# Performance work log

Hardware: AMD Instinct MI355X
Metric: run time of the kernel (lower is better)

The kernel has to match this reference:

```python
import jax, jax.numpy as jnp
import numpy as np

B, S, E, H, NE, K = 4, 1024, 1024, 16, 8, 2
DFF = 4 * E
DH = E // H
EPS = 1e-5


def _ln(x, g, b):
    m = jnp.mean(x, axis=-1, keepdims=True)
    v = jnp.mean(jnp.square(x - m), axis=-1, keepdims=True)
    return (x - m) * jax.lax.rsqrt(v + EPS) * g + b


def setup_inputs() -> dict:
    key = jax.random.key(0)
    ks = jax.random.split(key, 20)
    n = lambda k, sh, s: (jax.random.normal(k, sh, jnp.float32) * s)
    return {
        'x': n(ks[0], (B, S, E), 1.0),
        'ln1_g': jnp.ones((E,), jnp.float32), 'ln1_b': jnp.zeros((E,), jnp.float32),
        'wq': n(ks[1], (E, E), 0.02), 'bq': jnp.zeros((E,), jnp.float32),
        'wk': n(ks[2], (E, E), 0.02), 'bk': jnp.zeros((E,), jnp.float32),
        'wv': n(ks[3], (E, E), 0.02), 'bv': jnp.zeros((E,), jnp.float32),
        'wo': n(ks[4], (E, E), 0.02), 'bo': jnp.zeros((E,), jnp.float32),
        'ln2_g': jnp.ones((E,), jnp.float32), 'ln2_b': jnp.zeros((E,), jnp.float32),
        'sw1': n(ks[5], (E, DFF), 0.02), 'sb1': jnp.zeros((DFF,), jnp.float32),
        'sw2': n(ks[6], (DFF, E), 0.02), 'sb2': jnp.zeros((E,), jnp.float32),
        'ew1': n(ks[7], (NE, E, DFF), 0.02), 'eb1': jnp.zeros((NE, DFF), jnp.float32),
        'ew2': n(ks[8], (NE, DFF, E), 0.02), 'eb2': jnp.zeros((NE, E), jnp.float32),
        'w_gate': n(ks[9], (E, NE), 1.0),
    }


def reference(x, ln1_g, ln1_b, wq, bq, wk, bk, wv, bv, wo, bo,
              ln2_g, ln2_b, sw1, sb1, sw2, sb2, ew1, eb1, ew2, eb2, w_gate):
    # --- self-attention sublayer (eval: no dropout) ---
    res1 = x
    h = _ln(x, ln1_g, ln1_b)
    q = (h @ wq + bq).reshape(B, S, H, DH)
    k = (h @ wk + bk).reshape(B, S, H, DH)
    v = (h @ wv + bv).reshape(B, S, H, DH)
    scores = jnp.einsum('bqhd,bkhd->bhqk', q, k) / jnp.sqrt(jnp.float32(DH))
    attn = jax.nn.softmax(scores, axis=-1)
    ctx = jnp.einsum('bhqk,bkhd->bqhd', attn, v).reshape(B, S, E)
    x = res1 + (ctx @ wo + bo)

    # --- MoE sublayer ---
    res2 = x
    h2 = _ln(x, ln2_g, ln2_b)
    shared = jax.nn.gelu(h2 @ sw1 + sb1, approximate=False) @ sw2 + sb2

    # router (eval: clean logits, no noise)
    logits = h2 @ w_gate                                  # (B,S,NE)
    top_vals, top_idx = jax.lax.top_k(logits, K)          # (B,S,K)
    top_gates = jax.nn.softmax(top_vals, axis=-1)
    onehot = jax.nn.one_hot(top_idx, NE, dtype=x.dtype)   # (B,S,K,NE)
    gates = jnp.einsum('bsk,bske->bse', top_gates, onehot)
    probs = jax.nn.softmax(logits, axis=-1).reshape(-1, NE)
    P = probs.mean(0)
    f = (gates > 0).astype(x.dtype).reshape(-1, NE).mean(0)
    aux_loss = NE * jnp.sum(P * f)

    # dense all-expert compute, gated combine (matches original math)
    eh = jax.nn.gelu(jnp.einsum('bse,neh->bnsh', h2, ew1) + eb1[None, :, None, :],
                     approximate=False)
    eo = jnp.einsum('bnsh,nhe->bnse', eh, ew2) + eb2[None, :, None, :]
    expert_out = jnp.einsum('bnse,bsn->bse', eo, gates)

    return res2 + shared + expert_out, aux_loss
```

## Files before the change

### kernel.cpp

```cpp
#include <hip/hip_runtime.h>
#include <stdint.h>

#define B_    4
#define S_    1024
#define E_    1024
#define H_    16
#define NE_   8
#define DFF_  4096
#define NT_   4096
#define QS_   3072
#define ROWCAP_ 9216

typedef unsigned short u16;
typedef short bf16x8 __attribute__((ext_vector_type(8)));
typedef float f32x4 __attribute__((ext_vector_type(4)));

__device__ __forceinline__ float bf2f(u16 u){ unsigned v = ((unsigned)u) << 16; return __builtin_bit_cast(float, v); }
__device__ __forceinline__ u16 f2bf(float f){ unsigned x = __builtin_bit_cast(unsigned, f); return (u16)((x + 0x7FFFu + ((x >> 16) & 1u)) >> 16); }
__device__ __forceinline__ float gelu_f(float x){ return 0.5f * x * (1.f + erff(x * 0.70710678118f)); }

__device__ __forceinline__ void gl_lds16(const u16* g, u16* l){
  __builtin_amdgcn_global_load_lds((__attribute__((address_space(1))) void*)(const_cast<u16*>(g)),
                                   (__attribute__((address_space(3))) void*)(l), 16, 0, 0);
}

__launch_bounds__(256)
__global__ void ln_kernel(const float* __restrict__ x, const float* __restrict__ g,
                          const float* __restrict__ be, u16* __restrict__ out)
{
  const int row = blockIdx.x;
  const float4 v = ((const float4*)(x + (size_t)row * E_))[threadIdx.x];
  float s = v.x + v.y + v.z + v.w;
  #pragma unroll
  for(int mm = 32; mm >= 1; mm >>= 1) s += __shfl_xor(s, mm);
  __shared__ float red[8];
  const int wid = threadIdx.x >> 6;
  if((threadIdx.x & 63) == 0) red[wid] = s;
  __syncthreads();
  const float mean = (red[0] + red[1] + red[2] + red[3]) * (1.0f / E_);
  const float d0 = v.x - mean, d1 = v.y - mean, d2 = v.z - mean, d3 = v.w - mean;
  float q2 = d0*d0 + d1*d1 + d2*d2 + d3*d3;
  #pragma unroll
  for(int mm = 32; mm >= 1; mm >>= 1) q2 += __shfl_xor(q2, mm);
  if((threadIdx.x & 63) == 0) red[4 + wid] = q2;
  __syncthreads();
  const float var = (red[4] + red[5] + red[6] + red[7]) * (1.0f / E_);
  const float rs = rsqrtf(var + 1e-5f);
  const float4 gg = ((const float4*)g)[threadIdx.x];
  const float4 bb = ((const float4*)be)[threadIdx.x];
  ushort4 o;
  o.x = f2bf(d0 * rs * gg.x + bb.x);
  o.y = f2bf(d1 * rs * gg.y + bb.y);
  o.z = f2bf(d2 * rs * gg.z + bb.z);
  o.w = f2bf(d3 * rs * gg.w + bb.w);
  ((ushort4*)(out + (size_t)row * E_))[threadIdx.x] = o;
}

__launch_bounds__(256)
__global__ void transpose_kernel(const float* __restrict__ W, u16* __restrict__ WT, int K, int N)
{
  __shared__ __align__(16) u16 t[64][72];
  const size_t zo = (size_t)blockIdx.z * K * N;
  const int k0 = blockIdx.x * 64, n0 = blockIdx.y * 64;
  const int tid = threadIdx.x;
  const int kr = tid >> 2;
  const int nc = (tid & 3) * 4;
  #pragma unroll
  for(int p = 0; p < 4; p++){
    float4 v = *(const float4*)(W + zo + (size_t)(k0 + kr) * N + n0 + nc + p * 16);
    t[nc + p*16 + 0][kr] = f2bf(v.x);
    t[nc + p*16 + 1][kr] = f2bf(v.y);
    t[nc + p*16 + 2][kr] = f2bf(v.z);
    t[nc + p*16 + 3][kr] = f2bf(v.w);
  }
  __syncthreads();
  const int nr = tid >> 3;
  const int kg = (tid & 7) * 8;
  #pragma unroll
  for(int p = 0; p < 2; p++){
    const int nn = nr + p * 32;
    unsigned u0 = t[nn][kg+0], u1 = t[nn][kg+1], u2 = t[nn][kg+2], u3 = t[nn][kg+3];
    unsigned u4 = t[nn][kg+4], u5 = t[nn][kg+5], u6 = t[nn][kg+6], u7 = t[nn][kg+7];
    uint4 o;
    o.x = u0 | (u1 << 16); o.y = u2 | (u3 << 16); o.z = u4 | (u5 << 16); o.w = u6 | (u7 << 16);
    *(uint4*)(WT + zo + (size_t)(n0 + nn) * K + k0 + kg) = o;
  }
}

__global__ void bcat_kernel(const float* __restrict__ bq, const float* __restrict__ bk,
                            const float* __restrict__ bv, float* __restrict__ bcat)
{
  const int i = blockIdx.x * 256 + threadIdx.x;
  if(i < 1024) bcat[i] = bq[i];
  else if(i < 2048) bcat[i] = bk[i - 1024];
  else if(i < 3072) bcat[i] = bv[i - 2048];
}

template<int MODE>
__launch_bounds__(256)
__global__ void gemm_kernel(const u16* __restrict__ A, const u16* __restrict__ Bt,
                            int N, int Kd, const float* __restrict__ bias,
                            u16* __restrict__ outB)
{
  __shared__ __align__(16) u16 As0[4096], Bs0[4096], As1[4096], Bs1[4096];
  const int tid = threadIdx.x, lane = tid & 63, wid = tid >> 6;
  const int wm = wid >> 1, wn = wid & 1;
  const int tm = blockIdx.y * 128, tn = blockIdx.x * 128;

  const f32x4 zero = {0.f, 0.f, 0.f, 0.f};
  f32x4 acc[4][4];
  #pragma unroll
  for(int m = 0; m < 4; m++)
    #pragma unroll
    for(int n = 0; n < 4; n++) acc[m][n] = zero;

  const u16* gA0 = A  + (size_t)(tm + wid*32 + (lane >> 2)) * Kd + ((lane & 3) << 3);
  const u16* gA1 = gA0 + (size_t)16 * Kd;
  const u16* gB0 = Bt + (size_t)(tn + wid*32 + (lane >> 2)) * Kd + ((lane & 3) << 3);
  const u16* gB1 = gB0 + (size_t)16 * Kd;
  u16* lA0 = As0 + wid*1024; u16* lA1 = lA0 + 512;
  u16* lB0 = Bs0 + wid*1024; u16* lB1 = lB0 + 512;
  u16* lA0b = As1 + wid*1024; u16* lA1b = lA0b + 512;
  u16* lB0b = Bs1 + wid*1024; u16* lB1b = lB0b + 512;

  for(int k0 = 0; k0 < Kd; k0 += 64){
    __syncthreads();
    gl_lds16(gA0 + k0, lA0);  gl_lds16(gA1 + k0, lA1);
    gl_lds16(gB0 + k0, lB0);  gl_lds16(gB1 + k0, lB1);
    gl_lds16(gA0 + k0+32, lA0b); gl_lds16(gA1 + k0+32, lA1b);
    gl_lds16(gB0 + k0+32, lB0b); gl_lds16(gB1 + k0+32, lB1b);
    __syncthreads();
    bf16x8 aF[4], bF[4];
    #pragma unroll
    for(int m = 0; m < 4; m++) aF[m] = *(const bf16x8*)(As0 + (wm*64 + m*16 + (lane & 15)) * 32 + ((lane >> 4) << 3));
    #pragma unroll
    for(int n = 0; n < 4; n++) bF[n] = *(const bf16x8*)(Bs0 + (wn*64 + n*16 + (lane & 15)) * 32 + ((lane >> 4) << 3));
    #pragma unroll
    for(int m = 0; m < 4; m++)
      #pragma unroll
      for(int n = 0; n < 4; n++)
        acc[m][n] = __builtin_amdgcn_mfma_f32_16x16x32_bf16(aF[m], bF[n], acc[m][n], 0, 0, 0);
    #pragma unroll
    for(int m = 0; m < 4; m++) aF[m] = *(const bf16x8*)(As1 + (wm*64 + m*16 + (lane & 15)) * 32 + ((lane >> 4) << 3));
    #pragma unroll
    for(int n = 0; n < 4; n++) bF[n] = *(const bf16x8*)(Bs1 + (wn*64 + n*16 + (lane & 15)) * 32 + ((lane >> 4) << 3));
    #pragma unroll
    for(int m = 0; m < 4; m++)
      #pragma unroll
      for(int n = 0; n < 4; n++)
        acc[m][n] = __builtin_amdgcn_mfma_f32_16x16x32_bf16(aF[m], bF[n], acc[m][n], 0, 0, 0);
  }

  #pragma unroll
  for(int m = 0; m < 4; m++){
    const int row = tm + wm*64 + m*16 + ((lane >> 4) << 2);
    #pragma unroll
    for(int n = 0; n < 4; n++){
      const int col = tn + wn*64 + n*16 + (lane & 15);
      const float bc = bias[col];
      #pragma unroll
      for(int r = 0; r < 4; r++){
        const float v = acc[m][n][r] + bc;
        const size_t idx = (size_t)(row + r) * N + col;
        if constexpr(MODE == 0) outB[idx] = f2bf(v);
        else outB[idx] = f2bf(gelu_f(v));
      }
    }
  }
}

template<int MODE>
__launch_bounds__(256)
__global__ void gemm64_kernel(const u16* __restrict__ A, const u16* __restrict__ Bt,
                              int N, int Kd, const float* __restrict__ bias,
                              float* __restrict__ outF, const float* __restrict__ resid)
{
  __shared__ __align__(16) u16 As0[2048], As1[2048], Bs0[4096], Bs1[4096];
  const int tid = threadIdx.x, lane = tid & 63, wid = tid >> 6;
  const int wm = wid >> 1, wn = wid & 1;
  const int tm = blockIdx.y * 64, tn = blockIdx.x * 128;

  const f32x4 zero = {0.f, 0.f, 0.f, 0.f};
  f32x4 acc[2][4];
  #pragma unroll
  for(int m = 0; m < 2; m++)
    #pragma unroll
    for(int n = 0; n < 4; n++) acc[m][n] = zero;

  const u16* gA = A + (size_t)(tm + wid*16 + (lane >> 2)) * Kd + ((lane & 3) << 3);
  const u16* gB0 = Bt + (size_t)(tn + wid*32 + (lane >> 2)) * Kd + ((lane & 3) << 3);
  const u16* gB1 = gB0 + (size_t)16 * Kd;
  u16* lA  = As0 + wid*512;  u16* lAb = As1 + wid*512;
  u16* lB0 = Bs0 + wid*1024; u16* lB1 = lB0 + 512;
  u16* lB0b = Bs1 + wid*1024; u16* lB1b = lB0b + 512;

  for(int k0 = 0; k0 < Kd; k0 += 64){
    __syncthreads();
    gl_lds16(gA + k0, lA);
    gl_lds16(gB0 + k0, lB0); gl_lds16(gB1 + k0, lB1);
    gl_lds16(gA + k0+32, lAb);
    gl_lds16(gB0 + k0+32, lB0b); gl_lds16(gB1 + k0+32, lB1b);
    __syncthreads();
    bf16x8 aF[2], bF[4];
    #pragma unroll
    for(int m = 0; m < 2; m++) aF[m] = *(const bf16x8*)(As0 + (wm*32 + m*16 + (lane & 15)) * 32 + ((lane >> 4) << 3));
    #pragma unroll
    for(int n = 0; n < 4; n++) bF[n] = *(const bf16x8*)(Bs0 + (wn*64 + n*16 + (lane & 15)) * 32 + ((lane >> 4) << 3));
    #pragma unroll
    for(int m = 0; m < 2; m++)
      #pragma unroll
      for(int n = 0; n < 4; n++)
        acc[m][n] = __builtin_amdgcn_mfma_f32_16x16x32_bf16(aF[m], bF[n], acc[m][n], 0, 0, 0);
    #pragma unroll
    for(int m = 0; m < 2; m++) aF[m] = *(const bf16x8*)(As1 + (wm*32 + m*16 + (lane & 15)) * 32 + ((lane >> 4) << 3));
    #pragma unroll
    for(int n = 0; n < 4; n++) bF[n] = *(const bf16x8*)(Bs1 + (wn*64 + n*16 + (lane & 15)) * 32 + ((lane >> 4) << 3));
    #pragma unroll
    for(int m = 0; m < 2; m++)
      #pragma unroll
      for(int n = 0; n < 4; n++)
        acc[m][n] = __builtin_amdgcn_mfma_f32_16x16x32_bf16(aF[m], bF[n], acc[m][n], 0, 0, 0);
  }

  #pragma unroll
  for(int m = 0; m < 2; m++){
    const int row = tm + wm*32 + m*16 + ((lane >> 4) << 2);
    #pragma unroll
    for(int n = 0; n < 4; n++){
      const int col = tn + wn*64 + n*16 + (lane & 15);
      const float bc = bias[col];
      #pragma unroll
      for(int r = 0; r < 4; r++){
        const float v = acc[m][n][r] + bc;
        const size_t idx = (size_t)(row + r) * N + col;
        if constexpr(MODE == 2) outF[idx] = resid[idx] + v;
        else outF[idx] += v;
      }
    }
  }
}

__launch_bounds__(256)
__global__ void attn_kernel(const u16* __restrict__ qkv, u16* __restrict__ ctx)
{
  __shared__ __align__(16) u16 Ks[64 * 64];
  __shared__ __align__(16) u16 Vt[64 * 72];
  __shared__ __align__(16) u16 Ps[64 * 72];
  const int tid = threadIdx.x, lane = tid & 63, wid = tid >> 6;
  const int bh = blockIdx.y, bb = bh >> 4, hh = bh & 15;
  const int q0 = blockIdx.x * 64;
  const size_t tok0 = (size_t)bb * S_;
  const int hcol = hh * 64;

  bf16x8 aQ0, aQ1;
  {
    const u16* qp = qkv + (tok0 + q0 + wid*16 + (lane & 15)) * QS_ + hcol + ((lane >> 4) << 3);
    aQ0 = *(const bf16x8*)qp;
    aQ1 = *(const bf16x8*)(qp + 32);
  }
  const f32x4 zero = {0.f, 0.f, 0.f, 0.f};
  f32x4 accO[4]; float mrow[4], lrow[4];
  #pragma unroll
  for(int n = 0; n < 4; n++) accO[n] = zero;
  #pragma unroll
  for(int r = 0; r < 4; r++){ mrow[r] = -1e30f; lrow[r] = 0.f; }
  const float sc = 0.125f * 1.44269504f;

  for(int kv0 = 0; kv0 < S_; kv0 += 64){
    __syncthreads();
    {
      const u16* gp = qkv + (tok0 + kv0 + wid*16 + (lane >> 3)) * QS_ + 1024 + hcol + ((lane & 7) << 3);
      gl_lds16(gp, Ks + (wid*16) * 64);
      gl_lds16(gp + (size_t)8 * QS_, Ks + (wid*16 + 8) * 64);
    }
    {
      #pragma unroll
      for(int i = 0; i < 2; i++){
        const int tok = (tid >> 3) + i * 32;
        const int d0 = (tid & 7) << 3;
        bf16x8 vv = *(const bf16x8*)(qkv + (tok0 + kv0 + tok) * QS_ + 2048 + hcol + d0);
        #pragma unroll
        for(int j = 0; j < 8; j++) Vt[(d0 + j) * 72 + tok] = (u16)vv[j];
      }
    }
    __syncthreads();
    f32x4 sf[4];
    #pragma unroll
    for(int n = 0; n < 4; n++){
      bf16x8 b0 = *(const bf16x8*)(Ks + (n*16 + (lane & 15)) * 64 + ((lane >> 4) << 3));
      bf16x8 b1 = *(const bf16x8*)(Ks + (n*16 + (lane & 15)) * 64 + 32 + ((lane >> 4) << 3));
      f32x4 t = zero;
      t = __builtin_amdgcn_mfma_f32_16x16x32_bf16(aQ0, b0, t, 0, 0, 0);
      t = __builtin_amdgcn_mfma_f32_16x16x32_bf16(aQ1, b1, t, 0, 0, 0);
      sf[n] = t;
    }
    #pragma unroll
    for(int r = 0; r < 4; r++){
      const float s0 = sf[0][r]*sc, s1 = sf[1][r]*sc, s2 = sf[2][r]*sc, s3 = sf[3][r]*sc;
      float mx = fmaxf(fmaxf(s0, s1), fmaxf(s2, s3));
      #pragma unroll
      for(int mm = 1; mm < 16; mm <<= 1) mx = fmaxf(mx, __shfl_xor(mx, mm));
      const float mnew = fmaxf(mrow[r], mx);
      const float resc = exp2f(mrow[r] - mnew);
      mrow[r] = mnew;
      const float p0 = exp2f(s0 - mnew), p1 = exp2f(s1 - mnew);
      const float p2 = exp2f(s2 - mnew), p3 = exp2f(s3 - mnew);
      float ps = p0 + p1 + p2 + p3;
      #pragma unroll
      for(int mm = 1; mm < 16; mm <<= 1) ps += __shfl_xor(ps, mm);
      lrow[r] = lrow[r] * resc + ps;
      #pragma unroll
      for(int n = 0; n < 4; n++) accO[n][r] *= resc;
      const int prow = wid*16 + ((lane >> 4) << 2) + r;
      Ps[prow*72 +      (lane & 15)] = f2bf(p0);
      Ps[prow*72 + 16 + (lane & 15)] = f2bf(p1);
      Ps[prow*72 + 32 + (lane & 15)] = f2bf(p2);
      Ps[prow*72 + 48 + (lane & 15)] = f2bf(p3);
    }
    bf16x8 pa0 = *(const bf16x8*)(Ps + (wid*16 + (lane & 15)) * 72 + ((lane >> 4) << 3));
    bf16x8 pa1 = *(const bf16x8*)(Ps + (wid*16 + (lane & 15)) * 72 + 32 + ((lane >> 4) << 3));
    #pragma unroll
    for(int n = 0; n < 4; n++){
      bf16x8 b0 = *(const bf16x8*)(Vt + (n*16 + (lane & 15)) * 72 + ((lane >> 4) << 3));
      bf16x8 b1 = *(const bf16x8*)(Vt + (n*16 + (lane & 15)) * 72 + 32 + ((lane >> 4) << 3));
      accO[n] = __builtin_amdgcn_mfma_f32_16x16x32_bf16(pa0, b0, accO[n], 0, 0, 0);
      accO[n] = __builtin_amdgcn_mfma_f32_16x16x32_bf16(pa1, b1, accO[n], 0, 0, 0);
    }
  }
  const size_t cbase = tok0 * E_ + hcol;
  #pragma unroll
  for(int n = 0; n < 4; n++)
    #pragma unroll
    for(int r = 0; r < 4; r++){
      const int row = q0 + wid*16 + ((lane >> 4) << 2) + r;
      const int col = n*16 + (lane & 15);
      ctx[cbase + (size_t)row * E_ + col] = f2bf(accO[n][r] / lrow[r]);
    }
}

__launch_bounds__(256)
__global__ void router_kernel(const u16* __restrict__ h2, const float* __restrict__ wg,
                              float* __restrict__ probs, float* __restrict__ tkgate,
                              int* __restrict__ tkidx, int* __restrict__ counts)
{
  const int tok = blockIdx.x * 4 + (threadIdx.x >> 6);
  const int lane = threadIdx.x & 63;
  const u16* hr = h2 + (size_t)tok * E_;
  float a0=0,a1=0,a2=0,a3=0,a4=0,a5=0,a6=0,a7=0;
  for(int i0 = lane * 8; i0 < E_; i0 += 512){
    bf16x8 hv = *(const bf16x8*)(hr + i0);
    #pragma unroll
    for(int j = 0; j < 8; j++){
      const float hx = bf2f((u16)hv[j]);
      const float* wr = wg + (size_t)(i0 + j) * NE_;
      float4 w0 = *(const float4*)wr;
      float4 w1 = *(const float4*)(wr + 4);
      a0 += hx*w0.x; a1 += hx*w0.y; a2 += hx*w0.z; a3 += hx*w0.w;
      a4 += hx*w1.x; a5 += hx*w1.y; a6 += hx*w1.z; a7 += hx*w1.w;
    }
  }
  #pragma unroll
  for(int mm = 1; mm < 64; mm <<= 1){
    a0 += __shfl_xor(a0, mm); a1 += __shfl_xor(a1, mm); a2 += __shfl_xor(a2, mm); a3 += __shfl_xor(a3, mm);
    a4 += __shfl_xor(a4, mm); a5 += __shfl_xor(a5, mm); a6 += __shfl_xor(a6, mm); a7 += __shfl_xor(a7, mm);
  }
  if(lane == 0){
    float lg[8] = {a0,a1,a2,a3,a4,a5,a6,a7};
    float mx = lg[0];
    #pragma unroll
    for(int e = 1; e < 8; e++) mx = fmaxf(mx, lg[e]);
    float se = 0.f, ex[8];
    #pragma unroll
    for(int e = 0; e < 8; e++){ ex[e] = expf(lg[e] - mx); se += ex[e]; }
    const float inv = 1.f / se;
    float* pr = probs + (size_t)tok * 8;
    #pragma unroll
    for(int e = 0; e < 8; e++) pr[e] = ex[e] * inv;
    int i1 = 0; float v1 = lg[0];
    #pragma unroll
    for(int e = 1; e < 8; e++) if(lg[e] > v1){ v1 = lg[e]; i1 = e; }
    int i2 = -1; float v2 = -3.4e38f;
    #pragma unroll
    for(int e = 0; e < 8; e++) if(e != i1 && lg[e] > v2){ v2 = lg[e]; i2 = e; }
    const float t = expf(v2 - v1);
    tkidx[tok*2] = i1; tkidx[tok*2+1] = i2;
    tkgate[tok*2] = 1.f / (1.f + t); tkgate[tok*2+1] = t / (1.f + t);
    atomicAdd(&counts[i1], 1); atomicAdd(&counts[i2], 1);
  }
}

__global__ void init_kernel(int* __restrict__ counts, int* __restrict__ rowlist)
{
  const int t = blockIdx.x * 256 + threadIdx.x;
  if(t < 16) counts[t] = 0;
  if(t < ROWCAP_) rowlist[t] = -1;
}

__global__ void scan_kernel(const int* __restrict__ counts, int* __restrict__ aoff, int* __restrict__ cursor)
{
  if(threadIdx.x == 0){
    int o = 0;
    for(int e = 0; e < 8; e++){
      aoff[e] = o; cursor[e] = o;
      o += ((counts[e] + 127) >> 7) << 7;
    }
    aoff[8] = o;
  }
}

__global__ void build_kernel(const int* __restrict__ tkidx, const float* __restrict__ tkgate,
                             int* __restrict__ cursor, int* __restrict__ rowlist, float* __restrict__ rowgate)
{
  const int t = blockIdx.x * 256 + threadIdx.x;
  if(t >= NT_) return;
  #pragma unroll
  for(int kk = 0; kk < 2; kk++){
    const int e = tkidx[t*2 + kk];
    const int pos = atomicAdd(&cursor[e], 1);
    rowlist[pos] = t; rowgate[pos] = tkgate[t*2 + kk];
  }
}

__launch_bounds__(256)
__global__ void egemm1_kernel(const u16* __restrict__ Ah2, const u16* __restrict__ ewT,
                              const float* __restrict__ eb1,
                              const int* __restrict__ rowlist, const int* __restrict__ aoff,
                              u16* __restrict__ ehid)
{
  const int rowTile = blockIdx.y * 128;
  if(rowTile >= aoff[8]) return;
  int e = 0;
  #pragma unroll
  for(int i = 1; i < 8; i++) if(rowTile >= aoff[i]) e = i;
  __shared__ __align__(16) u16 As0[4096], Bs0[4096], As1[4096], Bs1[4096];
  const int tid = threadIdx.x, lane = tid & 63, wid = tid >> 6;
  const int wm = wid >> 1, wn = wid & 1;
  const int tn = blockIdx.x * 128;
  const u16* Bt = ewT + (size_t)e * DFF_ * E_;

  const int r0 = rowTile + wid*32 + (lane >> 2);
  int t0 = rowlist[r0];      if(t0 < 0) t0 = 0;
  int t1 = rowlist[r0 + 16]; if(t1 < 0) t1 = 0;
  const u16* gA0 = Ah2 + (size_t)t0 * E_ + ((lane & 3) << 3);
  const u16* gA1 = Ah2 + (size_t)t1 * E_ + ((lane & 3) << 3);
  const u16* gB0 = Bt + (size_t)(tn + wid*32 + (lane >> 2)) * E_ + ((lane & 3) << 3);
  const u16* gB1 = gB0 + (size_t)16 * E_;
  u16* lA0 = As0 + wid*1024; u16* lA1 = lA0 + 512;
  u16* lB0 = Bs0 + wid*1024; u16* lB1 = lB0 + 512;
  u16* lA0b = As1 + wid*1024; u16* lA1b = lA0b + 512;
  u16* lB0b = Bs1 + wid*1024; u16* lB1b = lB0b + 512;

  const f32x4 zero = {0.f,0.f,0.f,0.f};
  f32x4 acc[4][4];
  #pragma unroll
  for(int m = 0; m < 4; m++)
    #pragma unroll
    for(int n = 0; n < 4; n++) acc[m][n] = zero;

  for(int k0 = 0; k0 < E_; k0 += 64){
    __syncthreads();
    gl_lds16(gA0 + k0, lA0);  gl_lds16(gA1 + k0, lA1);
    gl_lds16(gB0 + k0, lB0);  gl_lds16(gB1 + k0, lB1);
    gl_lds16(gA0 + k0+32, lA0b); gl_lds16(gA1 + k0+32, lA1b);
    gl_lds16(gB0 + k0+32, lB0b); gl_lds16(gB1 + k0+32, lB1b);
    __syncthreads();
    bf16x8 aF[4], bF[4];
    #pragma unroll
    for(int m = 0; m < 4; m++) aF[m] = *(const bf16x8*)(As0 + (wm*64 + m*16 + (lane & 15)) * 32 + ((lane >> 4) << 3));
    #pragma unroll
    for(int n = 0; n < 4; n++) bF[n] = *(const bf16x8*)(Bs0 + (wn*64 + n*16 + (lane & 15)) * 32 + ((lane >> 4) << 3));
    #pragma unroll
    for(int m = 0; m < 4; m++)
      #pragma unroll
      for(int n = 0; n < 4; n++)
        acc[m][n] = __builtin_amdgcn_mfma_f32_16x16x32_bf16(aF[m], bF[n], acc[m][n], 0, 0, 0);
    #pragma unroll
    for(int m = 0; m < 4; m++) aF[m] = *(const bf16x8*)(As1 + (wm*64 + m*16 + (lane & 15)) * 32 + ((lane >> 4) << 3));
    #pragma unroll
    for(int n = 0; n < 4; n++) bF[n] = *(const bf16x8*)(Bs1 + (wn*64 + n*16 + (lane & 15)) * 32 + ((lane >> 4) << 3));
    #pragma unroll
    for(int m = 0; m < 4; m++)
      #pragma unroll
      for(int n = 0; n < 4; n++)
        acc[m][n] = __builtin_amdgcn_mfma_f32_16x16x32_bf16(aF[m], bF[n], acc[m][n], 0, 0, 0);
  }
  #pragma unroll
  for(int m = 0; m < 4; m++){
    const int row = rowTile + wm*64 + m*16 + ((lane >> 4) << 2);
    #pragma unroll
    for(int n = 0; n < 4; n++){
      const int col = tn + wn*64 + n*16 + (lane & 15);
      const float bc = eb1[e * DFF_ + col];
      #pragma unroll
      for(int r = 0; r < 4; r++)
        ehid[(size_t)(row + r) * DFF_ + col] = f2bf(gelu_f(acc[m][n][r] + bc));
    }
  }
}

__launch_bounds__(256)
__global__ void egemm2_kernel(const u16* __restrict__ ehid, const u16* __restrict__ ewT2,
                              const float* __restrict__ eb2,
                              const int* __restrict__ rowlist, const float* __restrict__ rowgate,
                              const int* __restrict__ aoff, float* __restrict__ outF)
{
  const int rowTile = blockIdx.y * 64;
  if(rowTile >= aoff[8]) return;
  int e = 0;
  #pragma unroll
  for(int i = 1; i < 8; i++) if(rowTile >= aoff[i]) e = i;
  __shared__ __align__(16) u16 As0[2048], As1[2048], Bs0[4096], Bs1[4096];
  const int tid = threadIdx.x, lane = tid & 63, wid = tid >> 6;
  const int wm = wid >> 1, wn = wid & 1;
  const int tn = blockIdx.x * 128;
  const u16* Bt = ewT2 + (size_t)e * E_ * DFF_;

  const u16* gA = ehid + (size_t)(rowTile + wid*16 + (lane >> 2)) * DFF_ + ((lane & 3) << 3);
  const u16* gB0 = Bt + (size_t)(tn + wid*32 + (lane >> 2)) * DFF_ + ((lane & 3) << 3);
  const u16* gB1 = gB0 + (size_t)16 * DFF_;
  u16* lA  = As0 + wid*512;  u16* lAb = As1 + wid*512;
  u16* lB0 = Bs0 + wid*1024; u16* lB1 = lB0 + 512;
  u16* lB0b = Bs1 + wid*1024; u16* lB1b = lB0b + 512;

  const f32x4 zero = {0.f,0.f,0.f,0.f};
  f32x4 acc[2][4];
  #pragma unroll
  for(int m = 0; m < 2; m++)
    #pragma unroll
    for(int n = 0; n < 4; n++) acc[m][n] = zero;

  for(int k0 = 0; k0 < DFF_; k0 += 64){
    __syncthreads();
    gl_lds16(gA + k0, lA);
    gl_lds16(gB0 + k0, lB0); gl_lds16(gB1 + k0, lB1);
    gl_lds16(gA + k0+32, lAb);
    gl_lds16(gB0 + k0+32, lB0b); gl_lds16(gB1 + k0+32, lB1b);
    __syncthreads();
    bf16x8 aF[2], bF[4];
    #pragma unroll
    for(int m = 0; m < 2; m++) aF[m] = *(const bf16x8*)(As0 + (wm*32 + m*16 + (lane & 15)) * 32 + ((lane >> 4) << 3));
    #pragma unroll
    for(int n = 0; n < 4; n++) bF[n] = *(const bf16x8*)(Bs0 + (wn*64 + n*16 + (lane & 15)) * 32 + ((lane >> 4) << 3));
    #pragma unroll
    for(int m = 0; m < 2; m++)
      #pragma unroll
      for(int n = 0; n < 4; n++)
        acc[m][n] = __builtin_amdgcn_mfma_f32_16x16x32_bf16(aF[m], bF[n], acc[m][n], 0, 0, 0);
    #pragma unroll
    for(int m = 0; m < 2; m++) aF[m] = *(const bf16x8*)(As1 + (wm*32 + m*16 + (lane & 15)) * 32 + ((lane >> 4) << 3));
    #pragma unroll
    for(int n = 0; n < 4; n++) bF[n] = *(const bf16x8*)(Bs1 + (wn*64 + n*16 + (lane & 15)) * 32 + ((lane >> 4) << 3));
    #pragma unroll
    for(int m = 0; m < 2; m++)
      #pragma unroll
      for(int n = 0; n < 4; n++)
        acc[m][n] = __builtin_amdgcn_mfma_f32_16x16x32_bf16(aF[m], bF[n], acc[m][n], 0, 0, 0);
  }
  #pragma unroll
  for(int m = 0; m < 2; m++){
    const int row = rowTile + wm*32 + m*16 + ((lane >> 4) << 2);
    #pragma unroll
    for(int r = 0; r < 4; r++){
      const int rr = row + r;
      const int tok = rowlist[rr];
      if(tok < 0) continue;
      const float g = rowgate[rr];
      #pragma unroll
      for(int n = 0; n < 4; n++){
        const int col = tn + wn*64 + n*16 + (lane & 15);
        atomicAdd(&outF[(size_t)tok * E_ + col], g * (acc[m][n][r] + eb2[e * E_ + col]));
      }
    }
  }
}

__launch_bounds__(256)
__global__ void aux_kernel(const float* __restrict__ probs, const int* __restrict__ counts,
                           float* __restrict__ outaux)
{
  float a[8];
  #pragma unroll
  for(int e = 0; e < 8; e++) a[e] = 0.f;
  for(int t = threadIdx.x; t < NT_; t += 256){
    const float* p = probs + (size_t)t * 8;
    #pragma unroll
    for(int e = 0; e < 8; e++) a[e] += p[e];
  }
  #pragma unroll
  for(int mm = 1; mm < 64; mm <<= 1)
    #pragma unroll
    for(int e = 0; e < 8; e++) a[e] += __shfl_xor(a[e], mm);
  __shared__ float part[4][8];
  const int wid = threadIdx.x >> 6;
  if((threadIdx.x & 63) == 0)
    for(int e = 0; e < 8; e++) part[wid][e] = a[e];
  __syncthreads();
  if(threadIdx.x == 0){
    float aux = 0.f;
    for(int e = 0; e < 8; e++){
      const float P = (part[0][e] + part[1][e] + part[2][e] + part[3][e]) / (float)NT_;
      const float f = (float)counts[e] / (float)NT_;
      aux += P * f;
    }
    outaux[0] = (float)NE_ * aux;
  }
}

extern "C" void kernel_launch(void* const* d_in, const int* in_sizes, int n_in,
                              void* d_out, int out_size, void* d_ws, size_t ws_size,
                              hipStream_t stream)
{
  (void)in_sizes; (void)n_in; (void)out_size; (void)ws_size;
  const float* x    = (const float*)d_in[0];
  const float* ln1g = (const float*)d_in[1];
  const float* ln1b = (const float*)d_in[2];
  const float* wq   = (const float*)d_in[3];
  const float* bq   = (const float*)d_in[4];
  const float* wk   = (const float*)d_in[5];
  const float* bk   = (const float*)d_in[6];
  const float* wv   = (const float*)d_in[7];
  const float* bv   = (const float*)d_in[8];
  const float* wo   = (const float*)d_in[9];
  const float* bo   = (const float*)d_in[10];
  const float* ln2g = (const float*)d_in[11];
  const float* ln2b = (const float*)d_in[12];
  const float* sw1  = (const float*)d_in[13];
  const float* sb1  = (const float*)d_in[14];
  const float* sw2  = (const float*)d_in[15];
  const float* sb2  = (const float*)d_in[16];
  const float* ew1  = (const float*)d_in[17];
  const float* eb1  = (const float*)d_in[18];
  const float* ew2  = (const float*)d_in[19];
  const float* eb2  = (const float*)d_in[20];
  const float* wgate= (const float*)d_in[21];
  float* out = (float*)d_out;
  char* ws = (char*)d_ws;

  const size_t MB = 1024ull * 1024ull;
  u16* h     = (u16*)(ws + 0);
  u16* h2    = (u16*)(ws + 8*MB);
  u16* wT    = (u16*)(ws + 16*MB);
  char* rt   = ws + 24*MB;
  float* probs   = (float*)(rt);
  float* tkgate  = (float*)(rt + 128*1024);
  int*   tkidx   = (int*)  (rt + 160*1024);
  int*   counts  = (int*)  (rt + 192*1024);
  int*   aoff    = (int*)  (rt + 192*1024 + 64);
  int*   cursor  = (int*)  (rt + 192*1024 + 128);
  int*   rowlist = (int*)  (rt + 256*1024);
  float* rowgate = (float*)(rt + 296*1024);
  float* bcat    = (float*)(rt + 512*1024);
  u16* qkvb  = (u16*)(ws + 32*MB);
  u16* ctx   = (u16*)(ws + 56*MB);
  u16* hidS  = (u16*)(ws + 64*MB);
  u16* ewT   = (u16*)(ws + 32*MB);
  u16* ehid  = (u16*)(ws + 96*MB);

  ln_kernel<<<NT_, 256, 0, stream>>>(x, ln1g, ln1b, h);
  bcat_kernel<<<12, 256, 0, stream>>>(bq, bk, bv, bcat);
  transpose_kernel<<<dim3(16,16,1), 256, 0, stream>>>(wq, wT,                 E_, E_);
  transpose_kernel<<<dim3(16,16,1), 256, 0, stream>>>(wk, wT + 1024*1024,     E_, E_);
  transpose_kernel<<<dim3(16,16,1), 256, 0, stream>>>(wv, wT + 2*1024*1024,   E_, E_);
  gemm_kernel<0><<<dim3(24,32), 256, 0, stream>>>(h, wT, QS_, E_, bcat, qkvb);
  attn_kernel<<<dim3(16,64), 256, 0, stream>>>(qkvb, ctx);
  transpose_kernel<<<dim3(16,16,1), 256, 0, stream>>>(wo, wT, E_, E_);
  gemm64_kernel<2><<<dim3(8,64), 256, 0, stream>>>(ctx, wT, E_, E_, bo, out, x);

  ln_kernel<<<NT_, 256, 0, stream>>>(out, ln2g, ln2b, h2);
  transpose_kernel<<<dim3(16,64,1), 256, 0, stream>>>(sw1, wT, E_, DFF_);
  gemm_kernel<1><<<dim3(32,32), 256, 0, stream>>>(h2, wT, DFF_, E_, sb1, hidS);
  transpose_kernel<<<dim3(64,16,1), 256, 0, stream>>>(sw2, wT, DFF_, E_);
  gemm64_kernel<3><<<dim3(8,64), 256, 0, stream>>>(hidS, wT, E_, DFF_, sb2, out, nullptr);

  init_kernel<<<36, 256, 0, stream>>>(counts, rowlist);
  router_kernel<<<1024, 256, 0, stream>>>(h2, wgate, probs, tkgate, tkidx, counts);
  scan_kernel<<<1, 64, 0, stream>>>(counts, aoff, cursor);
  build_kernel<<<16, 256, 0, stream>>>(tkidx, tkgate, cursor, rowlist, rowgate);

  transpose_kernel<<<dim3(16,64,8), 256, 0, stream>>>(ew1, ewT, E_, DFF_);
  egemm1_kernel<<<dim3(32,72), 256, 0, stream>>>(h2, ewT, eb1, rowlist, aoff, ehid);
  transpose_kernel<<<dim3(64,16,8), 256, 0, stream>>>(ew2, ewT, DFF_, E_);
  egemm2_kernel<<<dim3(8,144), 256, 0, stream>>>(ehid, ewT, eb2, rowlist, rowgate, aoff, out);

  aux_kernel<<<1, 256, 0, stream>>>(probs, counts, out + (size_t)NT_ * E_);
}
```

Before: 858.4 us.

## Double-buffer GEMM K-tiles with prefetch, XOR-swizzle LDS, fold init into prep

All four GEMM kernels move from loading two 32-wide K slices and then computing, with two barriers per step, to a ping-pong scheme. The next 32-wide K tile is prefetched into the alternate LDS buffer while the current one feeds the MFMAs, leaving one barrier per step. The global-to-LDS column offsets and the fragment reads get an XOR swizzle to reduce LDS bank conflicts, and the attention K tile gets the same treatment. The init kernel is merged into the bias-concat kernel, saving one launch. Correctness depends on the async global_load_lds finishing before the next iteration's barrier, with no explicit wait other than __syncthreads.

```diff
diff --git a/kernel.cpp b/kernel.cpp
--- a/kernel.cpp
+++ b/kernel.cpp
@@ -23,6 +23,9 @@
   __builtin_amdgcn_global_load_lds((__attribute__((address_space(1))) void*)(const_cast<u16*>(g)),
                                    (__attribute__((address_space(3))) void*)(l), 16, 0, 0);
 }
+
+#define KSW32(l)   ((((l) & 3) ^ (((l) >> 3) & 3)) << 3)
+#define FRAGOFF(l) (((l) & 15) * 32 + (((((l) >> 4) ^ (((l) >> 1) & 3))) << 3))
 
 __launch_bounds__(256)
 __global__ void ln_kernel(const float* __restrict__ x, const float* __restrict__ g,
@@ -87,13 +90,16 @@
   }
 }
 
-__global__ void bcat_kernel(const float* __restrict__ bq, const float* __restrict__ bk,
-                            const float* __restrict__ bv, float* __restrict__ bcat)
+__global__ void prep_kernel(const float* __restrict__ bq, const float* __restrict__ bk,
+                            const float* __restrict__ bv, float* __restrict__ bcat,
+                            int* __restrict__ counts, int* __restrict__ rowlist)
 {
   const int i = blockIdx.x * 256 + threadIdx.x;
   if(i < 1024) bcat[i] = bq[i];
   else if(i < 2048) bcat[i] = bk[i - 1024];
   else if(i < 3072) bcat[i] = bv[i - 2048];
+  if(i < 16) counts[i] = 0;
+  if(i < ROWCAP_) rowlist[i] = -1;
 }
 
 template<int MODE>
@@ -102,7 +108,7 @@
                             int N, int Kd, const float* __restrict__ bias,
                             u16* __restrict__ outB)
 {
-  __shared__ __align__(16) u16 As0[4096], Bs0[4096], As1[4096], Bs1[4096];
+  __shared__ __align__(16) u16 As[2][4096], Bs[2][4096];
   const int tid = threadIdx.x, lane = tid & 63, wid = tid >> 6;
   const int wm = wid >> 1, wn = wid & 1;
   const int tm = blockIdx.y * 128, tn = blockIdx.x * 128;
@@ -114,36 +120,35 @@
     #pragma unroll
     for(int n = 0; n < 4; n++) acc[m][n] = zero;
 
-  const u16* gA0 = A  + (size_t)(tm + wid*32 + (lane >> 2)) * Kd + ((lane & 3) << 3);
+  const int ksw = KSW32(lane);
+  const u16* gA0 = A  + (size_t)(tm + wid*32 + (lane >> 2)) * Kd + ksw;
   const u16* gA1 = gA0 + (size_t)16 * Kd;
-  const u16* gB0 = Bt + (size_t)(tn + wid*32 + (lane >> 2)) * Kd + ((lane & 3) << 3);
+  const u16* gB0 = Bt + (size_t)(tn + wid*32 + (lane >> 2)) * Kd + ksw;
   const u16* gB1 = gB0 + (size_t)16 * Kd;
-  u16* lA0 = As0 + wid*1024; u16* lA1 = lA0 + 512;
-  u16* lB0 = Bs0 + wid*1024; u16* lB1 = lB0 + 512;
-  u16* lA0b = As1 + wid*1024; u16* lA1b = lA0b + 512;
-  u16* lB0b = Bs1 + wid*1024; u16* lB1b = lB0b + 512;
-
-  for(int k0 = 0; k0 < Kd; k0 += 64){
+  const int seg = wid * 1024;
+
+  const int nt = Kd >> 5;
+  gl_lds16(gA0, &As[0][seg]); gl_lds16(gA1, &As[0][seg + 512]);
+  gl_lds16(gB0, &Bs[0][seg]); gl_lds16(gB1, &Bs[0][seg + 512]);
+
+  const int fo = FRAGOFF(lane);
+  const int fA = wm * 2048, fB = wn * 2048;
+
+  for(int t = 0; t < nt; ++t){
     __syncthreads();
-    gl_lds16(gA0 + k0, lA0);  gl_lds16(gA1 + k0, lA1);
-    gl_lds16(gB0 + k0, lB0);  gl_lds16(gB1 + k0, lB1);
-    gl_lds16(gA0 + k0+32, lA0b); gl_lds16(gA1 + k0+32, lA1b);
-    gl_lds16(gB0 + k0+32, lB0b); gl_lds16(gB1 + k0+32, lB1b);
-    __syncthreads();
+    if(t + 1 < nt){
+      const int ko = (t + 1) << 5;
+      const int b = (t + 1) & 1;
+      gl_lds16(gA0 + ko, &As[b][seg]); gl_lds16(gA1 + ko, &As[b][seg + 512]);
+      gl_lds16(gB0 + ko, &Bs[b][seg]); gl_lds16(gB1 + ko, &Bs[b][seg + 512]);
+    }
+    const u16* as = &As[t & 1][0];
+    const u16* bs = &Bs[t & 1][0];
     bf16x8 aF[4], bF[4];
     #pragma unroll
-    for(int m = 0; m < 4; m++) aF[m] = *(const bf16x8*)(As0 + (wm*64 + m*16 + (lane & 15)) * 32 + ((lane >> 4) << 3));
-    #pragma unroll
-    for(int n = 0; n < 4; n++) bF[n] = *(const bf16x8*)(Bs0 + (wn*64 + n*16 + (lane & 15)) * 32 + ((lane >> 4) << 3));
-    #pragma unroll
-    for(int m = 0; m < 4; m++)
-      #pragma unroll
-      for(int n = 0; n < 4; n++)
-        acc[m][n] = __builtin_amdgcn_mfma_f32_16x16x32_bf16(aF[m], bF[n], acc[m][n], 0, 0, 0);
-    #pragma unroll
-    for(int m = 0; m < 4; m++) aF[m] = *(const bf16x8*)(As1 + (wm*64 + m*16 + (lane & 15)) * 32 + ((lane >> 4) << 3));
-    #pragma unroll
-    for(int n = 0; n < 4; n++) bF[n] = *(const bf16x8*)(Bs1 + (wn*64 + n*16 + (lane & 15)) * 32 + ((lane >> 4) << 3));
+    for(int m = 0; m < 4; m++) aF[m] = *(const bf16x8*)(as + fA + m*512 + fo);
+    #pragma unroll
+    for(int n = 0; n < 4; n++) bF[n] = *(const bf16x8*)(bs + fB + n*512 + fo);
     #pragma unroll
     for(int m = 0; m < 4; m++)
       #pragma unroll
@@ -175,7 +180,7 @@
                               int N, int Kd, const float* __restrict__ bias,
                               float* __restrict__ outF, const float* __restrict__ resid)
 {
-  __shared__ __align__(16) u16 As0[2048], As1[2048], Bs0[4096], Bs1[4096];
+  __shared__ __align__(16) u16 As[2][2048], Bs[2][4096];
   const int tid = threadIdx.x, lane = tid & 63, wid = tid >> 6;
   const int wm = wid >> 1, wn = wid & 1;
   const int tm = blockIdx.y * 64, tn = blockIdx.x * 128;
@@ -187,34 +192,34 @@
     #pragma unroll
     for(int n = 0; n < 4; n++) acc[m][n] = zero;
 
-  const u16* gA = A + (size_t)(tm + wid*16 + (lane >> 2)) * Kd + ((lane & 3) << 3);
-  const u16* gB0 = Bt + (size_t)(tn + wid*32 + (lane >> 2)) * Kd + ((lane & 3) << 3);
+  const int ksw = KSW32(lane);
+  const u16* gA = A + (size_t)(tm + wid*16 + (lane >> 2)) * Kd + ksw;
+  const u16* gB0 = Bt + (size_t)(tn + wid*32 + (lane >> 2)) * Kd + ksw;
   const u16* gB1 = gB0 + (size_t)16 * Kd;
-  u16* lA  = As0 + wid*512;  u16* lAb = As1 + wid*512;
-  u16* lB0 = Bs0 + wid*1024; u16* lB1 = lB0 + 512;
-  u16* lB0b = Bs1 + wid*1024; u16* lB1b = lB0b + 512;
-
-  for(int k0 = 0; k0 < Kd; k0 += 64){
+  const int segA = wid * 512, segB = wid * 1024;
+
+  const int nt = Kd >> 5;
+  gl_lds16(gA, &As[0][segA]);
+  gl_lds16(gB0, &Bs[0][segB]); gl_lds16(gB1, &Bs[0][segB + 512]);
+
+  const int fo = FRAGOFF(lane);
+  const int fA = wm * 1024, fB = wn * 2048;
+
+  for(int t = 0; t < nt; ++t){
     __syncthreads();
-    gl_lds16(gA + k0, lA);
-    gl_lds16(gB0 + k0, lB0); gl_lds16(gB1 + k0, lB1);
-    gl_lds16(gA + k0+32, lAb);
-    gl_lds16(gB0 + k0+32, lB0b); gl_lds16(gB1 + k0+32, lB1b);
-    __syncthreads();
+    if(t + 1 < nt){
+      const int ko = (t + 1) << 5;
+      const int b = (t + 1) & 1;
+      gl_lds16(gA + ko, &As[b][segA]);
+      gl_lds16(gB0 + ko, &Bs[b][segB]); gl_lds16(gB1 + ko, &Bs[b][segB + 512]);
+    }
+    const u16* as = &As[t & 1][0];
+    const u16* bs = &Bs[t & 1][0];
     bf16x8 aF[2], bF[4];
     #pragma unroll
-    for(int m = 0; m < 2; m++) aF[m] = *(const bf16x8*)(As0 + (wm*32 + m*16 + (lane & 15)) * 32 + ((lane >> 4) << 3));
-    #pragma unroll
-    for(int n = 0; n < 4; n++) bF[n] = *(const bf16x8*)(Bs0 + (wn*64 + n*16 + (lane & 15)) * 32 + ((lane >> 4) << 3));
-    #pragma unroll
-    for(int m = 0; m < 2; m++)
-      #pragma unroll
-      for(int n = 0; n < 4; n++)
-        acc[m][n] = __builtin_amdgcn_mfma_f32_16x16x32_bf16(aF[m], bF[n], acc[m][n], 0, 0, 0);
-    #pragma unroll
-    for(int m = 0; m < 2; m++) aF[m] = *(const bf16x8*)(As1 + (wm*32 + m*16 + (lane & 15)) * 32 + ((lane >> 4) << 3));
-    #pragma unroll
-    for(int n = 0; n < 4; n++) bF[n] = *(const bf16x8*)(Bs1 + (wn*64 + n*16 + (lane & 15)) * 32 + ((lane >> 4) << 3));
+    for(int m = 0; m < 2; m++) aF[m] = *(const bf16x8*)(as + fA + m*512 + fo);
+    #pragma unroll
+    for(int n = 0; n < 4; n++) bF[n] = *(const bf16x8*)(bs + fB + n*512 + fo);
     #pragma unroll
     for(int m = 0; m < 2; m++)
       #pragma unroll
@@ -265,11 +270,12 @@
   #pragma unroll
   for(int r = 0; r < 4; r++){ mrow[r] = -1e30f; lrow[r] = 0.f; }
   const float sc = 0.125f * 1.44269504f;
+  const int ksw8 = (((lane & 7) ^ ((lane >> 3) & 7)) << 3);
 
   for(int kv0 = 0; kv0 < S_; kv0 += 64){
     __syncthreads();
     {
-      const u16* gp = qkv + (tok0 + kv0 + wid*16 + (lane >> 3)) * QS_ + 1024 + hcol + ((lane & 7) << 3);
+      const u16* gp = qkv + (tok0 + kv0 + wid*16 + (lane >> 3)) * QS_ + 1024 + hcol + ksw8;
       gl_lds16(gp, Ks + (wid*16) * 64);
       gl_lds16(gp + (size_t)8 * QS_, Ks + (wid*16 + 8) * 64);
     }
@@ -287,8 +293,9 @@
     f32x4 sf[4];
     #pragma unroll
     for(int n = 0; n < 4; n++){
-      bf16x8 b0 = *(const bf16x8*)(Ks + (n*16 + (lane & 15)) * 64 + ((lane >> 4) << 3));
-      bf16x8 b1 = *(const bf16x8*)(Ks + (n*16 + (lane & 15)) * 64 + 32 + ((lane >> 4) << 3));
+      const int rb = n*16 + (lane & 15);
+      bf16x8 b0 = *(const bf16x8*)(Ks + rb*64 + ((((lane >> 4)    ) ^ (lane & 7)) << 3));
+      bf16x8 b1 = *(const bf16x8*)(Ks + rb*64 + ((((lane >> 4) + 4) ^ (lane & 7)) << 3));
       f32x4 t = zero;
       t = __builtin_amdgcn_mfma_f32_16x16x32_bf16(aQ0, b0, t, 0, 0, 0);
       t = __builtin_amdgcn_mfma_f32_16x16x32_bf16(aQ1, b1, t, 0, 0, 0);
@@ -389,13 +396,6 @@
   }
 }
 
-__global__ void init_kernel(int* __restrict__ counts, int* __restrict__ rowlist)
-{
-  const int t = blockIdx.x * 256 + threadIdx.x;
-  if(t < 16) counts[t] = 0;
-  if(t < ROWCAP_) rowlist[t] = -1;
-}
-
 __global__ void scan_kernel(const int* __restrict__ counts, int* __restrict__ aoff, int* __restrict__ cursor)
 {
   if(threadIdx.x == 0){
@@ -432,7 +432,7 @@
   int e = 0;
   #pragma unroll
   for(int i = 1; i < 8; i++) if(rowTile >= aoff[i]) e = i;
-  __shared__ __align__(16) u16 As0[4096], Bs0[4096], As1[4096], Bs1[4096];
+  __shared__ __align__(16) u16 As[2][4096], Bs[2][4096];
   const int tid = threadIdx.x, lane = tid & 63, wid = tid >> 6;
   const int wm = wid >> 1, wn = wid & 1;
   const int tn = blockIdx.x * 128;
@@ -441,14 +441,12 @@
   const int r0 = rowTile + wid*32 + (lane >> 2);
   int t0 = rowlist[r0];      if(t0 < 0) t0 = 0;
   int t1 = rowlist[r0 + 16]; if(t1 < 0) t1 = 0;
-  const u16* gA0 = Ah2 + (size_t)t0 * E_ + ((lane & 3) << 3);
-  const u16* gA1 = Ah2 + (size_t)t1 * E_ + ((lane & 3) << 3);
-  const u16* gB0 = Bt + (size_t)(tn + wid*32 + (lane >> 2)) * E_ + ((lane & 3) << 3);
+  const int ksw = KSW32(lane);
+  const u16* gA0 = Ah2 + (size_t)t0 * E_ + ksw;
+  const u16* gA1 = Ah2 + (size_t)t1 * E_ + ksw;
+  const u16* gB0 = Bt + (size_t)(tn + wid*32 + (lane >> 2)) * E_ + ksw;
   const u16* gB1 = gB0 + (size_t)16 * E_;
-  u16* lA0 = As0 + wid*1024; u16* lA1 = lA0 + 512;
-  u16* lB0 = Bs0 + wid*1024; u16* lB1 = lB0 + 512;
-  u16* lA0b = As1 + wid*1024; u16* lA1b = lA0b + 512;
-  u16* lB0b = Bs1 + wid*1024; u16* lB1b = lB0b + 512;
+  const int seg = wid * 1024;
 
   const f32x4 zero = {0.f,0.f,0.f,0.f};
   f32x4 acc[4][4];
@@ -457,27 +455,28 @@
     #pragma unroll
     for(int n = 0; n < 4; n++) acc[m][n] = zero;
 
-  for(int k0 = 0; k0 < E_; k0 += 64){
+  gl_lds16(gA0, &As[0][seg]); gl_lds16(gA1, &As[0][seg + 512]);
+  gl_lds16(gB0, &Bs[0][seg]); gl_lds16(gB1, &Bs[0][seg + 512]);
+
+  const int fo = FRAGOFF(lane);
+  const int fA = wm * 2048, fB = wn * 2048;
+  const int nt = E_ >> 5;
+
+  for(int t = 0; t < nt; ++t){
     __syncthreads();
-    gl_lds16(gA0 + k0, lA0);  gl_lds16(gA1 + k0, lA1);
-    gl_lds16(gB0 + k0, lB0);  gl_lds16(gB1 + k0, lB1);
-    gl_lds16(gA0 + k0+32, lA0b); gl_lds16(gA1 + k0+32, lA1b);
-    gl_lds16(gB0 + k0+32, lB0b); gl_lds16(gB1 + k0+32, lB1b);
-    __syncthreads();
+    if(t + 1 < nt){
+      const int ko = (t + 1) << 5;
+      const int b = (t + 1) & 1;
+      gl_lds16(gA0 + ko, &As[b][seg]); gl_lds16(gA1 + ko, &As[b][seg + 512]);
+      gl_lds16(gB0 + ko, &Bs[b][seg]); gl_lds16(gB1 + ko, &Bs[b][seg + 512]);
+    }
+    const u16* as = &As[t & 1][0];
+    const u16* bs = &Bs[t & 1][0];
     bf16x8 aF[4], bF[4];
     #pragma unroll
-    for(int m = 0; m < 4; m++) aF[m] = *(const bf16x8*)(As0 + (wm*64 + m*16 + (lane & 15)) * 32 + ((lane >> 4) << 3));
-    #pragma unroll
-    for(int n = 0; n < 4; n++) bF[n] = *(const bf16x8*)(Bs0 + (wn*64 + n*16 + (lane & 15)) * 32 + ((lane >> 4) << 3));
-    #pragma unroll
-    for(int m = 0; m < 4; m++)
-      #pragma unroll
-      for(int n = 0; n < 4; n++)
-        acc[m][n] = __builtin_amdgcn_mfma_f32_16x16x32_bf16(aF[m], bF[n], acc[m][n], 0, 0, 0);
-    #pragma unroll
-    for(int m = 0; m < 4; m++) aF[m] = *(const bf16x8*)(As1 + (wm*64 + m*16 + (lane & 15)) * 32 + ((lane >> 4) << 3));
-    #pragma unroll
-    for(int n = 0; n < 4; n++) bF[n] = *(const bf16x8*)(Bs1 + (wn*64 + n*16 + (lane & 15)) * 32 + ((lane >> 4) << 3));
+    for(int m = 0; m < 4; m++) aF[m] = *(const bf16x8*)(as + fA + m*512 + fo);
+    #pragma unroll
+    for(int n = 0; n < 4; n++) bF[n] = *(const bf16x8*)(bs + fB + n*512 + fo);
     #pragma unroll
     for(int m = 0; m < 4; m++)
       #pragma unroll
@@ -509,18 +508,17 @@
   int e = 0;
   #pragma unroll
   for(int i = 1; i < 8; i++) if(rowTile >= aoff[i]) e = i;
-  __shared__ __align__(16) u16 As0[2048], As1[2048], Bs0[4096], Bs1[4096];
+  __shared__ __align__(16) u16 As[2][2048], Bs[2][4096];
   const int tid = threadIdx.x, lane = tid & 63, wid = tid >> 6;
   const int wm = wid >> 1, wn = wid & 1;
   const int tn = blockIdx.x * 128;
   const u16* Bt = ewT2 + (size_t)e * E_ * DFF_;
 
-  const u16* gA = ehid + (size_t)(rowTile + wid*16 + (lane >> 2)) * DFF_ + ((lane & 3) << 3);
-  const u16* gB0 = Bt + (size_t)(tn + wid*32 + (lane >> 2)) * DFF_ + ((lane & 3) << 3);
+  const int ksw = KSW32(lane);
+  const u16* gA = ehid + (size_t)(rowTile + wid*16 + (lane >> 2)) * DFF_ + ksw;
+  const u16* gB0 = Bt + (size_t)(tn + wid*32 + (lane >> 2)) * DFF_ + ksw;
   const u16* gB1 = gB0 + (size_t)16 * DFF_;
-  u16* lA  = As0 + wid*512;  u16* lAb = As1 + wid*512;
-  u16* lB0 = Bs0 + wid*1024; u16* lB1 = lB0 + 512;
-  u16* lB0b = Bs1 + wid*1024; u16* lB1b = lB0b + 512;
+  const int segA = wid * 512, segB = wid * 1024;
 
   const f32x4 zero = {0.f,0.f,0.f,0.f};
   f32x4 acc[2][4];
@@ -529,27 +527,28 @@
     #pragma unroll
     for(int n = 0; n < 4; n++) acc[m][n] = zero;
 
-  for(int k0 = 0; k0 < DFF_; k0 += 64){
+  gl_lds16(gA, &As[0][segA]);
+  gl_lds16(gB0, &Bs[0][segB]); gl_lds16(gB1, &Bs[0][segB + 512]);
+
+  const int fo = FRAGOFF(lane);
+  const int fA = wm * 1024, fB = wn * 2048;
+  const int nt = DFF_ >> 5;
+
+  for(int t = 0; t < nt; ++t){
     __syncthreads();
-    gl_lds16(gA + k0, lA);
-    gl_lds16(gB0 + k0, lB0); gl_lds16(gB1 + k0, lB1);
-    gl_lds16(gA + k0+32, lAb);
-    gl_lds16(gB0 + k0+32, lB0b); gl_lds16(gB1 + k0+32, lB1b);
-    __syncthreads();
+    if(t + 1 < nt){
+      const int ko = (t + 1) << 5;
+      const int b = (t + 1) & 1;
+      gl_lds16(gA + ko, &As[b][segA]);
+      gl_lds16(gB0 + ko, &Bs[b][segB]); gl_lds16(gB1 + ko, &Bs[b][segB + 512]);
+    }
+    const u16* as = &As[t & 1][0];
+    const u16* bs = &Bs[t & 1][0];
     bf16x8 aF[2], bF[4];
     #pragma unroll
-    for(int m = 0; m < 2; m++) aF[m] = *(const bf16x8*)(As0 + (wm*32 + m*16 + (lane & 15)) * 32 + ((lane >> 4) << 3));
-    #pragma unroll
-    for(int n = 0; n < 4; n++) bF[n] = *(const bf16x8*)(Bs0 + (wn*64 + n*16 + (lane & 15)) * 32 + ((lane >> 4) << 3));
-    #pragma unroll
-    for(int m = 0; m < 2; m++)
-      #pragma unroll
-      for(int n = 0; n < 4; n++)
-        acc[m][n] = __builtin_amdgcn_mfma_f32_16x16x32_bf16(aF[m], bF[n], acc[m][n], 0, 0, 0);
-    #pragma unroll
-    for(int m = 0; m < 2; m++) aF[m] = *(const bf16x8*)(As1 + (wm*32 + m*16 + (lane & 15)) * 32 + ((lane >> 4) << 3));
-    #pragma unroll
-    for(int n = 0; n < 4; n++) bF[n] = *(const bf16x8*)(Bs1 + (wn*64 + n*16 + (lane & 15)) * 32 + ((lane >> 4) << 3));
+    for(int m = 0; m < 2; m++) aF[m] = *(const bf16x8*)(as + fA + m*512 + fo);
+    #pragma unroll
+    for(int n = 0; n < 4; n++) bF[n] = *(const bf16x8*)(bs + fB + n*512 + fo);
     #pragma unroll
     for(int m = 0; m < 2; m++)
       #pragma unroll
@@ -657,7 +656,7 @@
   u16* ehid  = (u16*)(ws + 96*MB);
 
   ln_kernel<<<NT_, 256, 0, stream>>>(x, ln1g, ln1b, h);
-  bcat_kernel<<<12, 256, 0, stream>>>(bq, bk, bv, bcat);
+  prep_kernel<<<36, 256, 0, stream>>>(bq, bk, bv, bcat, counts, rowlist);
   transpose_kernel<<<dim3(16,16,1), 256, 0, stream>>>(wq, wT,                 E_, E_);
   transpose_kernel<<<dim3(16,16,1), 256, 0, stream>>>(wk, wT + 1024*1024,     E_, E_);
   transpose_kernel<<<dim3(16,16,1), 256, 0, stream>>>(wv, wT + 2*1024*1024,   E_, E_);
@@ -672,7 +671,6 @@
   transpose_kernel<<<dim3(64,16,1), 256, 0, stream>>>(sw2, wT, DFF_, E_);
   gemm64_kernel<3><<<dim3(8,64), 256, 0, stream>>>(hidS, wT, E_, DFF_, sb2, out, nullptr);
 
-  init_kernel<<<36, 256, 0, stream>>>(counts, rowlist);
   router_kernel<<<1024, 256, 0, stream>>>(h2, wgate, probs, tkgate, tkidx, counts);
   scan_kernel<<<1, 64, 0, stream>>>(counts, aoff, cursor);
   build_kernel<<<16, 256, 0, stream>>>(tkidx, tkgate, cursor, rowlist, rowgate);
```

Result: no change. 845.3 us (-1.5%).
